# Kernel optimization log

Measured on AMD Instinct MI355X. Metric: run time of the kernel, lower is better.

Reference implementation:

```python
import jax, jax.numpy as jnp
import numpy as np

B, S, H, NH = 2, 2048, 1024, 16
HD = H // NH  # 64


def setup_inputs() -> dict:
    key = jax.random.key(0)
    ks = jax.random.split(key, 9)
    w = lambda k: jax.random.normal(k, (H, H), dtype=jnp.float32) * 0.02  # torch Linear weight [out,in]
    b = lambda k: jax.random.normal(k, (H,), dtype=jnp.float32) * 0.02
    return {
        "hidden_states": jax.random.normal(ks[0], (B, S, H), dtype=jnp.float32),
        "Wq": w(ks[1]), "bq": b(ks[2]),
        "Wk": w(ks[3]), "bk": b(ks[4]),
        "Wv": w(ks[5]), "bv": b(ks[6]),
        "Wo": w(ks[7]), "bo": b(ks[8]),
    }


def reference(hidden_states, Wq, bq, Wk, bk, Wv, bv, Wo, bo):
    b, s, h = hidden_states.shape
    nh, hd = NH, h // NH

    def proj(W, bias):
        y = hidden_states @ W.T + bias  # torch Linear: x W^T + b
        return y.reshape(b, s, nh, hd).transpose(0, 2, 1, 3)  # [b, h, s, d]

    q = proj(Wq, bq)
    k = proj(Wk, bk)
    v = proj(Wv, bv)

    scale = jnp.sqrt(jnp.asarray(hd, dtype=q.dtype))
    scores = jnp.einsum("bhqd,bhkd->bhqk", q, k) / scale  # [b, h, s, s]
    pos = jnp.arange(s)
    causal = pos[:, None] < pos[None, :]  # True where masked (key after query)
    scores = jnp.where(causal[None, None], -jnp.inf, scores)
    attn = jax.nn.softmax(scores, axis=-1)
    out = jnp.einsum("bhqk,bhkd->bhqd", attn, v)
    out = out.transpose(0, 2, 1, 3).reshape(b, s, h)
    return out @ Wo.T + bo
```

## Files before the change

kernel.cpp:

```cpp
#include <hip/hip_runtime.h>
#include <stdint.h>

typedef __bf16 bf16;
typedef __attribute__((ext_vector_type(2))) __bf16 bf16x2;
typedef __attribute__((ext_vector_type(4))) __bf16 bf16x4;
typedef __attribute__((ext_vector_type(8))) __bf16 bf16x8;
typedef __attribute__((ext_vector_type(4))) float f32x4;
typedef __attribute__((ext_vector_type(4))) short s16x4;

#define B_  2
#define S_  2048
#define H_  1024
#define NH_ 16
#define HD_ 64

__device__ __forceinline__ void glds16(const bf16* g, bf16* l) {
  __builtin_amdgcn_global_load_lds(
      (const __attribute__((address_space(1))) uint32_t*)g,
      (__attribute__((address_space(3))) uint32_t*)l, 16, 0, 0);
}

__device__ __forceinline__ f32x4 pv_mfma(bf16x4 a, bf16x4 b, f32x4 c) {
#if __has_builtin(__builtin_amdgcn_mfma_f32_16x16x16bf16_1k)
  union U { bf16x4 h; s16x4 s; };
  U ua; ua.h = a;
  U ub; ub.h = b;
  return __builtin_amdgcn_mfma_f32_16x16x16bf16_1k(ua.s, ub.s, c, 0, 0, 0);
#else
  f32x4 d;
  asm volatile("v_mfma_f32_16x16x16_bf16 %0, %1, %2, %3\n\ts_nop 7\n\ts_nop 7"
               : "=v"(d) : "v"(a), "v"(b), "v"(c));
  return d;
#endif
}

__global__ __launch_bounds__(256) void cvt_f32_bf16(
    const float* __restrict__ s0, bf16* __restrict__ d0, int n0,
    const float* __restrict__ s1, bf16* __restrict__ d1,
    const float* __restrict__ s2, bf16* __restrict__ d2,
    const float* __restrict__ s3, bf16* __restrict__ d3,
    const float* __restrict__ s4, bf16* __restrict__ d4, int nw)
{
  const float* s; bf16* d; int n;
  switch (blockIdx.y) {
    case 0:  s = s0; d = d0; n = n0; break;
    case 1:  s = s1; d = d1; n = nw; break;
    case 2:  s = s2; d = d2; n = nw; break;
    case 3:  s = s3; d = d3; n = nw; break;
    default: s = s4; d = d4; n = nw; break;
  }
  const int i = (blockIdx.x * 256 + threadIdx.x) * 8;
  if (i >= n) return;
  float4 v0 = *(const float4*)(s + i);
  float4 v1 = *(const float4*)(s + i + 4);
  bf16x8 o;
  o[0] = (bf16)v0.x; o[1] = (bf16)v0.y; o[2] = (bf16)v0.z; o[3] = (bf16)v0.w;
  o[4] = (bf16)v1.x; o[5] = (bf16)v1.y; o[6] = (bf16)v1.z; o[7] = (bf16)v1.w;
  *(bf16x8*)(d + i) = o;
}

__global__ __launch_bounds__(256) void gemm_qkv(
    const bf16* __restrict__ X,
    const bf16* __restrict__ W0, const bf16* __restrict__ W1, const bf16* __restrict__ W2,
    const float* __restrict__ b0, const float* __restrict__ b1, const float* __restrict__ b2,
    bf16* __restrict__ Y0, bf16* __restrict__ Y1, bf16* __restrict__ Y2,
    float ys0, int M, int N, int K)
{
  const bf16* W; const float* bias; bf16* Y; float ysc;
  if (blockIdx.z == 0)      { W = W0; bias = b0; Y = Y0; ysc = ys0; }
  else if (blockIdx.z == 1) { W = W1; bias = b1; Y = Y1; ysc = 1.0f; }
  else                      { W = W2; bias = b2; Y = Y2; ysc = 1.0f; }

  __shared__ __align__(16) bf16 As[2][128 * 32];
  __shared__ __align__(16) bf16 Bs[2][128 * 32];

  const int tid  = threadIdx.x;
  const int lane = tid & 63;
  const int wave = tid >> 6;
  const int m0 = blockIdx.y * 128;
  const int n0 = blockIdx.x * 128;
  const int wm = (wave >> 1) * 64;
  const int wn = (wave & 1) * 64;

  const int r0 = tid >> 2,            c0 = (tid & 3) * 8;
  const int r1 = (256 + tid) >> 2,    c1 = ((256 + tid) & 3) * 8;
  const int cb0 = (wave * 64) * 8;
  const int cb1 = (256 + wave * 64) * 8;

  f32x4 acc[4][4] = {};

  glds16(X + (size_t)(m0 + r0) * K + c0, &As[0][cb0]);
  glds16(W + (size_t)(n0 + r0) * K + c0, &Bs[0][cb0]);
  glds16(X + (size_t)(m0 + r1) * K + c1, &As[0][cb1]);
  glds16(W + (size_t)(n0 + r1) * K + c1, &Bs[0][cb1]);

  int pb = 0;
  for (int k0 = 0; k0 < K; k0 += 32, pb ^= 1) {
    __syncthreads();

    if (k0 + 32 < K) {
      const int kn = k0 + 32;
      glds16(X + (size_t)(m0 + r0) * K + kn + c0, &As[pb ^ 1][cb0]);
      glds16(W + (size_t)(n0 + r0) * K + kn + c0, &Bs[pb ^ 1][cb0]);
      glds16(X + (size_t)(m0 + r1) * K + kn + c1, &As[pb ^ 1][cb1]);
      glds16(W + (size_t)(n0 + r1) * K + kn + c1, &Bs[pb ^ 1][cb1]);
    }

    bf16x8 a[4], b[4];
#pragma unroll
    for (int i = 0; i < 4; ++i)
      a[i] = *(const bf16x8*)&As[pb][(wm + i * 16 + (lane & 15)) * 32 + (lane >> 4) * 8];
#pragma unroll
    for (int i = 0; i < 4; ++i)
      b[i] = *(const bf16x8*)&Bs[pb][(wn + i * 16 + (lane & 15)) * 32 + (lane >> 4) * 8];
#pragma unroll
    for (int mi = 0; mi < 4; ++mi)
#pragma unroll
      for (int ni = 0; ni < 4; ++ni)
        acc[mi][ni] = __builtin_amdgcn_mfma_f32_16x16x32_bf16(a[mi], b[ni], acc[mi][ni], 0, 0, 0);
  }

#pragma unroll
  for (int mi = 0; mi < 4; ++mi) {
    const int row = m0 + wm + mi * 16 + (lane >> 4) * 4;
#pragma unroll
    for (int ni = 0; ni < 4; ++ni) {
      const int col = n0 + wn + ni * 16 + (lane & 15);
      const float bv = bias[col];
#pragma unroll
      for (int r = 0; r < 4; ++r)
        Y[(size_t)(row + r) * N + col] = (bf16)((acc[mi][ni][r] + bv) * ysc);
    }
  }
}

__global__ __launch_bounds__(256) void gemm_o_64(
    const bf16* __restrict__ X, const bf16* __restrict__ W,
    const float* __restrict__ bias, float* __restrict__ Y)
{
  constexpr int K = 1024, N = 1024;
  __shared__ __align__(16) bf16 As[2][64 * 32];
  __shared__ __align__(16) bf16 Bs[2][128 * 32];

  const int tid  = threadIdx.x;
  const int lane = tid & 63;
  const int wave = tid >> 6;
  const int m0 = blockIdx.y * 64;
  const int n0 = blockIdx.x * 128;
  const int wm = (wave >> 1) * 32;
  const int wn = (wave & 1) * 64;

  const int ar = tid >> 2,  ac = (tid & 3) * 8;
  const int br0 = tid >> 2,          bc0 = (tid & 3) * 8;
  const int br1 = (256 + tid) >> 2,  bc1 = ((256 + tid) & 3) * 8;
  const int acb  = (wave * 64) * 8;
  const int bcb0 = (wave * 64) * 8;
  const int bcb1 = (256 + wave * 64) * 8;

  f32x4 acc[2][4] = {};

  glds16(X + (size_t)(m0 + ar) * K + ac,   &As[0][acb]);
  glds16(W + (size_t)(n0 + br0) * K + bc0, &Bs[0][bcb0]);
  glds16(W + (size_t)(n0 + br1) * K + bc1, &Bs[0][bcb1]);

  int pb = 0;
  for (int k0 = 0; k0 < K; k0 += 32, pb ^= 1) {
    __syncthreads();

    if (k0 + 32 < K) {
      const int kn = k0 + 32;
      glds16(X + (size_t)(m0 + ar) * K + kn + ac,   &As[pb ^ 1][acb]);
      glds16(W + (size_t)(n0 + br0) * K + kn + bc0, &Bs[pb ^ 1][bcb0]);
      glds16(W + (size_t)(n0 + br1) * K + kn + bc1, &Bs[pb ^ 1][bcb1]);
    }

    bf16x8 a[2], b[4];
#pragma unroll
    for (int i = 0; i < 2; ++i)
      a[i] = *(const bf16x8*)&As[pb][(wm + i * 16 + (lane & 15)) * 32 + (lane >> 4) * 8];
#pragma unroll
    for (int i = 0; i < 4; ++i)
      b[i] = *(const bf16x8*)&Bs[pb][(wn + i * 16 + (lane & 15)) * 32 + (lane >> 4) * 8];
#pragma unroll
    for (int mi = 0; mi < 2; ++mi)
#pragma unroll
      for (int ni = 0; ni < 4; ++ni)
        acc[mi][ni] = __builtin_amdgcn_mfma_f32_16x16x32_bf16(a[mi], b[ni], acc[mi][ni], 0, 0, 0);
  }

#pragma unroll
  for (int mi = 0; mi < 2; ++mi) {
    const int row = m0 + wm + mi * 16 + (lane >> 4) * 4;
#pragma unroll
    for (int ni = 0; ni < 4; ++ni) {
      const int col = n0 + wn + ni * 16 + (lane & 15);
      const float bv = bias[col];
#pragma unroll
      for (int r = 0; r < 4; ++r)
        Y[(size_t)(row + r) * N + col] = acc[mi][ni][r] + bv;
    }
  }
}

__device__ __forceinline__ void attn_tile_step(
    const bf16* Ksb, const bf16* Vtb, const bf16x8 bq[2], int qrow, int k0,
    bool maskit, float& mr, float& lr, f32x4 oacc[4], int l15, int quad)
{
  f32x4 sacc[8] = {};
  __builtin_amdgcn_s_setprio(1);
#pragma unroll
  for (int ks = 0; ks < 2; ++ks) {
#pragma unroll
    for (int mb = 0; mb < 8; ++mb) {
      const int row = mb * 16 + l15;
      const int ch  = (ks * 4 + quad) ^ (l15 & 7);
      bf16x8 ak = *(const bf16x8*)&Ksb[row * 64 + ch * 8];
      sacc[mb] = __builtin_amdgcn_mfma_f32_16x16x32_bf16(ak, bq[ks], sacc[mb], 0, 0, 0);
    }
  }
  __builtin_amdgcn_s_setprio(0);

  if (maskit) {
#pragma unroll
    for (int mb = 0; mb < 8; ++mb) {
      const int kb = k0 + mb * 16 + quad * 4;
#pragma unroll
      for (int r = 0; r < 4; ++r)
        if (kb + r > qrow) sacc[mb][r] = -1e30f;
    }
  }

  float mx = -1e30f;
#pragma unroll
  for (int mb = 0; mb < 8; ++mb)
    mx = fmaxf(mx, fmaxf(fmaxf(sacc[mb][0], sacc[mb][1]),
                         fmaxf(sacc[mb][2], sacc[mb][3])));
  mx = fmaxf(mx, __shfl_xor(mx, 16, 64));
  mx = fmaxf(mx, __shfl_xor(mx, 32, 64));

  float sum = 0.0f;
  bf16x4 pwv[8];
#pragma unroll
  for (int mb = 0; mb < 8; ++mb) {
    bf16x4 pw;
#pragma unroll
    for (int r = 0; r < 4; ++r) {
      const float p = __builtin_amdgcn_exp2f(sacc[mb][r] - mr);
      sum += p;
      pw[r] = (bf16)p;
    }
    pwv[mb] = pw;
  }
  sum += __shfl_xor(sum, 16, 64);
  sum += __shfl_xor(sum, 32, 64);

  __builtin_amdgcn_s_setprio(1);
#pragma unroll
  for (int mb = 0; mb < 8; ++mb) {
#pragma unroll
    for (int db = 0; db < 4; ++db) {
      const int vch = ((mb * 4 + quad) ^ (l15 & 7)) * 4;
      bf16x4 av = *(const bf16x4*)&Vtb[(db * 16 + l15) * 128 + vch];
      oacc[db] = pv_mfma(av, pwv[mb], oacc[db]);
    }
  }
  __builtin_amdgcn_s_setprio(0);

  lr += sum;
  if (!__all(mx <= mr + 8.0f)) {
    const float mnew  = fmaxf(mr, mx);
    const float alpha = __builtin_amdgcn_exp2f(mr - mnew);
    lr *= alpha;
#pragma unroll
    for (int db = 0; db < 4; ++db)
#pragma unroll
      for (int r = 0; r < 4; ++r) oacc[db][r] *= alpha;
    mr = mnew;
  }
}

__global__ __launch_bounds__(256, 2) void attn_causal(
    const bf16* __restrict__ Q, const bf16* __restrict__ K,
    const bf16* __restrict__ V, bf16* __restrict__ O)
{
  const int lin  = blockIdx.x;
  const int slot = lin >> 3;
  const int bh   = (lin & 7) * 4 + (slot >> 4);
  const int pair = slot & 15;
  const int b    = bh >> 4;
  const int h    = bh & 15;

  const int tid  = threadIdx.x;
  const int lane = tid & 63;
  const int wave = tid >> 6;
  const int quad = lane >> 4;
  const int l15  = lane & 15;
  const size_t headoff = (size_t)b * S_ * H_ + (size_t)h * HD_;
  const bf16* Kp = K + headoff;
  const bf16* Vp = V + headoff;

  __shared__ __align__(16) bf16 Ks[2][128 * 64];
  __shared__ __align__(16) bf16 Vt[2][64 * 128];

  const int qlo = pair, qhi = 31 - pair;
  const int nl  = (qlo >> 1) + 1;
  const int nh  = (qhi >> 1) + 1;
  const int qrowL = qlo * 64 + wave * 16 + l15;
  const int qrowH = qhi * 64 + wave * 16 + l15;

  bf16x8 bqL[2], bqH[2];
  bqL[0] = *(const bf16x8*)(Q + headoff + (size_t)qrowL * H_ + quad * 8);
  bqL[1] = *(const bf16x8*)(Q + headoff + (size_t)qrowL * H_ + 32 + quad * 8);
  bqH[0] = *(const bf16x8*)(Q + headoff + (size_t)qrowH * H_ + quad * 8);
  bqH[1] = *(const bf16x8*)(Q + headoff + (size_t)qrowH * H_ + 32 + quad * 8);

  const int vr = lane * 2;
  const int vc = wave * 16;

#define STAGE_K(k0_, buf_)                                                  \
  {                                                                         \
    _Pragma("unroll")                                                       \
    for (int j = 0; j < 4; ++j) {                                           \
      const int n = j * 256 + tid;                                          \
      const int row = n >> 3;                                               \
      const int cg  = (n & 7) ^ (row & 7);                                  \
      glds16(Kp + (size_t)((k0_) + row) * H_ + cg * 8,                      \
             &Ks[buf_][(j * 256 + wave * 64) * 8]);                         \
    }                                                                       \
  }

#define LOAD_V(k0_)                                                         \
  {                                                                         \
    vreg[0] = *(const bf16x8*)(Vp + (size_t)((k0_) + vr) * H_ + vc);        \
    vreg[1] = *(const bf16x8*)(Vp + (size_t)((k0_) + vr) * H_ + vc + 8);    \
    vreg[2] = *(const bf16x8*)(Vp + (size_t)((k0_) + vr + 1) * H_ + vc);    \
    vreg[3] = *(const bf16x8*)(Vp + (size_t)((k0_) + vr + 1) * H_ + vc + 8);\
  }

#define WRITE_V(buf_)                                                       \
  {                                                                         \
    _Pragma("unroll")                                                       \
    for (int e = 0; e < 8; ++e) {                                           \
      const int sw = (((vr >> 2) ^ e) * 4) + (vr & 3);                      \
      bf16x2 p0; p0[0] = vreg[0][e]; p0[1] = vreg[2][e];                    \
      *(bf16x2*)&Vt[buf_][(vc + e) * 128 + sw] = p0;                        \
      bf16x2 p1; p1[0] = vreg[1][e]; p1[1] = vreg[3][e];                    \
      *(bf16x2*)&Vt[buf_][(vc + 8 + e) * 128 + sw] = p1;                    \
    }                                                                       \
  }

  bf16x8 vreg[4];

  STAGE_K(0, 0);
  LOAD_V(0);
  WRITE_V(0);
  __syncthreads();

  float mrL = 0.0f, lrL = 0.0f, mrH = 0.0f, lrH = 0.0f;
  f32x4 oL[4] = {}, oH[4] = {};

  for (int it = 0; it < nh; ++it) {
    const int c = it & 1;
    const bool pre = (it + 1 < nh);

    if (pre) {
      STAGE_K((it + 1) * 128, c ^ 1);
      LOAD_V((it + 1) * 128);
    }

    attn_tile_step(Ks[c], Vt[c], bqH, qrowH, it * 128, it == nh - 1,
                   mrH, lrH, oH, l15, quad);
    if (it < nl)
      attn_tile_step(Ks[c], Vt[c], bqL, qrowL, it * 128, it == nl - 1,
                     mrL, lrL, oL, l15, quad);

    if (pre) {
      WRITE_V(c ^ 1);
      __syncthreads();
    }
  }

  const float invL = 1.0f / lrL;
#pragma unroll
  for (int db = 0; db < 4; ++db) {
    bf16x4 o;
#pragma unroll
    for (int r = 0; r < 4; ++r) o[r] = (bf16)(oL[db][r] * invL);
    *(bf16x4*)(O + headoff + (size_t)qrowL * H_ + db * 16 + quad * 4) = o;
  }
  const float invH = 1.0f / lrH;
#pragma unroll
  for (int db = 0; db < 4; ++db) {
    bf16x4 o;
#pragma unroll
    for (int r = 0; r < 4; ++r) o[r] = (bf16)(oH[db][r] * invH);
    *(bf16x4*)(O + headoff + (size_t)qrowH * H_ + db * 16 + quad * 4) = o;
  }
#undef STAGE_K
#undef LOAD_V
#undef WRITE_V
}

extern "C" void kernel_launch(void* const* d_in, const int* in_sizes, int n_in,
                              void* d_out, int out_size, void* d_ws, size_t ws_size,
                              hipStream_t stream) {
  const float* hs = (const float*)d_in[0];
  const float* Wq = (const float*)d_in[1]; const float* bq = (const float*)d_in[2];
  const float* Wk = (const float*)d_in[3]; const float* bk = (const float*)d_in[4];
  const float* Wv = (const float*)d_in[5]; const float* bv = (const float*)d_in[6];
  const float* Wo = (const float*)d_in[7]; const float* bo = (const float*)d_in[8];
  float* out = (float*)d_out;

  const size_t elems = (size_t)B_ * S_ * H_;
  const size_t wel   = (size_t)H_ * H_;
  bf16* hsb = (bf16*)d_ws;
  bf16* AO  = hsb;
  bf16* Wqb = hsb + elems;
  bf16* Wkb = Wqb + wel;
  bf16* Wvb = Wkb + wel;
  bf16* Wob = Wvb + wel;
  bf16* Qw  = Wob + wel;
  bf16* Kw  = Qw + elems;
  bf16* Vw  = Kw + elems;

  cvt_f32_bf16<<<dim3(2048, 5), dim3(256), 0, stream>>>(
      hs, hsb, (int)elems, Wq, Wqb, Wk, Wkb, Wv, Wvb, Wo, Wob, (int)wel);

  const int M = B_ * S_;
  const float QSCL = 0.125f * 1.44269504f;

  gemm_qkv<<<dim3(H_ / 128, M / 128, 3), dim3(256), 0, stream>>>(
      hsb, Wqb, Wkb, Wvb, bq, bk, bv, Qw, Kw, Vw, QSCL, M, H_, H_);

  attn_causal<<<dim3(512), dim3(256), 0, stream>>>(Qw, Kw, Vw, AO);

  gemm_o_64<<<dim3(8, 64), dim3(256), 0, stream>>>(AO, Wob, bo, out);
}
```

Measured before the change: 199.0 us.

## Fuse all four stages into one cooperative persistent kernel with grid syncs

Merges the conversion, QKV projection, causal attention and output projection into a single cooperatively launched kernel of 512 blocks, separated by grid-wide barriers. This removes three kernel launch boundaries and their tail gaps. The cost is that every phase must use one block count, one 64 KB shared-memory allocation and one register budget, and the QKV GEMM runs unevenly at 768 tiles over 512 blocks. If the cooperative launch fails, it falls back to four separate kernels.

```diff
diff --git a/kernel.cpp b/kernel.cpp
--- a/kernel.cpp
+++ b/kernel.cpp
@@ -1,5 +1,8 @@
 #include <hip/hip_runtime.h>
+#include <hip/hip_cooperative_groups.h>
 #include <stdint.h>
+
+namespace cg = cooperative_groups;
 
 typedef __bf16 bf16;
 typedef __attribute__((ext_vector_type(2))) __bf16 bf16x2;
@@ -13,6 +16,7 @@
 #define H_  1024
 #define NH_ 16
 #define HD_ 64
+#define QSCL_ (0.125f * 1.44269504f)
 
 __device__ __forceinline__ void glds16(const bf16* g, bf16* l) {
   __builtin_amdgcn_global_load_lds(
@@ -34,85 +38,92 @@
 #endif
 }
 
-__global__ __launch_bounds__(256) void cvt_f32_bf16(
-    const float* __restrict__ s0, bf16* __restrict__ d0, int n0,
-    const float* __restrict__ s1, bf16* __restrict__ d1,
-    const float* __restrict__ s2, bf16* __restrict__ d2,
-    const float* __restrict__ s3, bf16* __restrict__ d3,
-    const float* __restrict__ s4, bf16* __restrict__ d4, int nw)
-{
-  const float* s; bf16* d; int n;
-  switch (blockIdx.y) {
-    case 0:  s = s0; d = d0; n = n0; break;
-    case 1:  s = s1; d = d1; n = nw; break;
-    case 2:  s = s2; d = d2; n = nw; break;
-    case 3:  s = s3; d = d3; n = nw; break;
-    default: s = s4; d = d4; n = nw; break;
-  }
-  const int i = (blockIdx.x * 256 + threadIdx.x) * 8;
-  if (i >= n) return;
-  float4 v0 = *(const float4*)(s + i);
-  float4 v1 = *(const float4*)(s + i + 4);
+__device__ __forceinline__ bf16x8 cvt8(const float4 a, const float4 b) {
   bf16x8 o;
-  o[0] = (bf16)v0.x; o[1] = (bf16)v0.y; o[2] = (bf16)v0.z; o[3] = (bf16)v0.w;
-  o[4] = (bf16)v1.x; o[5] = (bf16)v1.y; o[6] = (bf16)v1.z; o[7] = (bf16)v1.w;
-  *(bf16x8*)(d + i) = o;
-}
-
-__global__ __launch_bounds__(256) void gemm_qkv(
+  o[0] = (bf16)a.x; o[1] = (bf16)a.y; o[2] = (bf16)a.z; o[3] = (bf16)a.w;
+  o[4] = (bf16)b.x; o[5] = (bf16)b.y; o[6] = (bf16)b.z; o[7] = (bf16)b.w;
+  return o;
+}
+
+
+__device__ __forceinline__ void cvt_phase(
+    int blk, int tid,
+    const float* __restrict__ hs, const float* __restrict__ Wq,
+    const float* __restrict__ Wk, const float* __restrict__ Wv,
+    const float* __restrict__ Wo,
+    bf16* __restrict__ hsb, bf16* __restrict__ Wqb, bf16* __restrict__ Wkb,
+    bf16* __restrict__ Wvb, bf16* __restrict__ Wob)
+{
+  const int g = blk * 256 + tid;
+#pragma unroll
+  for (int j = 0; j < 4; ++j) {
+    const size_t i = ((size_t)g + (size_t)j * 131072) * 8;
+    float4 a = *(const float4*)(hs + i), b = *(const float4*)(hs + i + 4);
+    *(bf16x8*)(hsb + i) = cvt8(a, b);
+  }
+  const size_t i = (size_t)g * 8;
+  { float4 a = *(const float4*)(Wq + i), b = *(const float4*)(Wq + i + 4);
+    *(bf16x8*)(Wqb + i) = cvt8(a, b); }
+  { float4 a = *(const float4*)(Wk + i), b = *(const float4*)(Wk + i + 4);
+    *(bf16x8*)(Wkb + i) = cvt8(a, b); }
+  { float4 a = *(const float4*)(Wv + i), b = *(const float4*)(Wv + i + 4);
+    *(bf16x8*)(Wvb + i) = cvt8(a, b); }
+  { float4 a = *(const float4*)(Wo + i), b = *(const float4*)(Wo + i + 4);
+    *(bf16x8*)(Wob + i) = cvt8(a, b); }
+}
+
+__device__ __forceinline__ void qkv_tile(
+    int z, int by, int bx, int tid, bf16* __restrict__ SM,
     const bf16* __restrict__ X,
     const bf16* __restrict__ W0, const bf16* __restrict__ W1, const bf16* __restrict__ W2,
     const float* __restrict__ b0, const float* __restrict__ b1, const float* __restrict__ b2,
-    bf16* __restrict__ Y0, bf16* __restrict__ Y1, bf16* __restrict__ Y2,
-    float ys0, int M, int N, int K)
-{
+    bf16* __restrict__ Y0, bf16* __restrict__ Y1, bf16* __restrict__ Y2)
+{
+  constexpr int K = 1024, N = 1024;
   const bf16* W; const float* bias; bf16* Y; float ysc;
-  if (blockIdx.z == 0)      { W = W0; bias = b0; Y = Y0; ysc = ys0; }
-  else if (blockIdx.z == 1) { W = W1; bias = b1; Y = Y1; ysc = 1.0f; }
-  else                      { W = W2; bias = b2; Y = Y2; ysc = 1.0f; }
-
-  __shared__ __align__(16) bf16 As[2][128 * 32];
-  __shared__ __align__(16) bf16 Bs[2][128 * 32];
-
-  const int tid  = threadIdx.x;
-  const int lane = tid & 63;
-  const int wave = tid >> 6;
-  const int m0 = blockIdx.y * 128;
-  const int n0 = blockIdx.x * 128;
-  const int wm = (wave >> 1) * 64;
-  const int wn = (wave & 1) * 64;
-
-  const int r0 = tid >> 2,            c0 = (tid & 3) * 8;
-  const int r1 = (256 + tid) >> 2,    c1 = ((256 + tid) & 3) * 8;
-  const int cb0 = (wave * 64) * 8;
-  const int cb1 = (256 + wave * 64) * 8;
+  if (z == 0)      { W = W0; bias = b0; Y = Y0; ysc = QSCL_; }
+  else if (z == 1) { W = W1; bias = b1; Y = Y1; ysc = 1.0f; }
+  else             { W = W2; bias = b2; Y = Y2; ysc = 1.0f; }
+
+  const int lane = tid & 63, wave = tid >> 6;
+  const int m0 = by * 128, n0 = bx * 128;
+  const int wm = (wave >> 1) * 64, wn = (wave & 1) * 64;
+  const int r0 = tid >> 2,         c0 = (tid & 3) * 8;
+  const int r1 = (256 + tid) >> 2, c1 = ((256 + tid) & 3) * 8;
+  const int cb0 = (wave * 64) * 8, cb1 = (256 + wave * 64) * 8;
+
+  bf16* As = SM;
+  bf16* Bs = SM + 8192;
 
   f32x4 acc[4][4] = {};
 
-  glds16(X + (size_t)(m0 + r0) * K + c0, &As[0][cb0]);
-  glds16(W + (size_t)(n0 + r0) * K + c0, &Bs[0][cb0]);
-  glds16(X + (size_t)(m0 + r1) * K + c1, &As[0][cb1]);
-  glds16(W + (size_t)(n0 + r1) * K + c1, &Bs[0][cb1]);
+  __syncthreads();
+  glds16(X + (size_t)(m0 + r0) * K + c0, As + cb0);
+  glds16(W + (size_t)(n0 + r0) * K + c0, Bs + cb0);
+  glds16(X + (size_t)(m0 + r1) * K + c1, As + cb1);
+  glds16(W + (size_t)(n0 + r1) * K + c1, Bs + cb1);
 
   int pb = 0;
   for (int k0 = 0; k0 < K; k0 += 32, pb ^= 1) {
     __syncthreads();
-
     if (k0 + 32 < K) {
       const int kn = k0 + 32;
-      glds16(X + (size_t)(m0 + r0) * K + kn + c0, &As[pb ^ 1][cb0]);
-      glds16(W + (size_t)(n0 + r0) * K + kn + c0, &Bs[pb ^ 1][cb0]);
-      glds16(X + (size_t)(m0 + r1) * K + kn + c1, &As[pb ^ 1][cb1]);
-      glds16(W + (size_t)(n0 + r1) * K + kn + c1, &Bs[pb ^ 1][cb1]);
-    }
-
+      bf16* An = As + (pb ^ 1) * 4096;
+      bf16* Bn = Bs + (pb ^ 1) * 4096;
+      glds16(X + (size_t)(m0 + r0) * K + kn + c0, An + cb0);
+      glds16(W + (size_t)(n0 + r0) * K + kn + c0, Bn + cb0);
+      glds16(X + (size_t)(m0 + r1) * K + kn + c1, An + cb1);
+      glds16(W + (size_t)(n0 + r1) * K + kn + c1, Bn + cb1);
+    }
+    const bf16* Ac = As + pb * 4096;
+    const bf16* Bc = Bs + pb * 4096;
     bf16x8 a[4], b[4];
 #pragma unroll
-    for (int i = 0; i < 4; ++i)
-      a[i] = *(const bf16x8*)&As[pb][(wm + i * 16 + (lane & 15)) * 32 + (lane >> 4) * 8];
-#pragma unroll
-    for (int i = 0; i < 4; ++i)
-      b[i] = *(const bf16x8*)&Bs[pb][(wn + i * 16 + (lane & 15)) * 32 + (lane >> 4) * 8];
+    for (int j = 0; j < 4; ++j)
+      a[j] = *(const bf16x8*)&Ac[(wm + j * 16 + (lane & 15)) * 32 + (lane >> 4) * 8];
+#pragma unroll
+    for (int j = 0; j < 4; ++j)
+      b[j] = *(const bf16x8*)&Bc[(wn + j * 16 + (lane & 15)) * 32 + (lane >> 4) * 8];
 #pragma unroll
     for (int mi = 0; mi < 4; ++mi)
 #pragma unroll
@@ -134,22 +145,16 @@
   }
 }
 
-__global__ __launch_bounds__(256) void gemm_o_64(
+__device__ __forceinline__ void o_tile(
+    int t, int tid, bf16* __restrict__ SM,
     const bf16* __restrict__ X, const bf16* __restrict__ W,
     const float* __restrict__ bias, float* __restrict__ Y)
 {
   constexpr int K = 1024, N = 1024;
-  __shared__ __align__(16) bf16 As[2][64 * 32];
-  __shared__ __align__(16) bf16 Bs[2][128 * 32];
-
-  const int tid  = threadIdx.x;
-  const int lane = tid & 63;
-  const int wave = tid >> 6;
-  const int m0 = blockIdx.y * 64;
-  const int n0 = blockIdx.x * 128;
-  const int wm = (wave >> 1) * 32;
-  const int wn = (wave & 1) * 64;
-
+  const int lane = tid & 63, wave = tid >> 6;
+  const int m0 = (t >> 3) * 64;
+  const int n0 = (t & 7) * 128;
+  const int wm = (wave >> 1) * 32, wn = (wave & 1) * 64;
   const int ar = tid >> 2,  ac = (tid & 3) * 8;
   const int br0 = tid >> 2,          bc0 = (tid & 3) * 8;
   const int br1 = (256 + tid) >> 2,  bc1 = ((256 + tid) & 3) * 8;
@@ -157,30 +162,36 @@
   const int bcb0 = (wave * 64) * 8;
   const int bcb1 = (256 + wave * 64) * 8;
 
+  bf16* As = SM;
+  bf16* Bs = SM + 4096;
+
   f32x4 acc[2][4] = {};
 
-  glds16(X + (size_t)(m0 + ar) * K + ac,   &As[0][acb]);
-  glds16(W + (size_t)(n0 + br0) * K + bc0, &Bs[0][bcb0]);
-  glds16(W + (size_t)(n0 + br1) * K + bc1, &Bs[0][bcb1]);
+  __syncthreads();
+  glds16(X + (size_t)(m0 + ar) * K + ac,   As + acb);
+  glds16(W + (size_t)(n0 + br0) * K + bc0, Bs + bcb0);
+  glds16(W + (size_t)(n0 + br1) * K + bc1, Bs + bcb1);
 
   int pb = 0;
   for (int k0 = 0; k0 < K; k0 += 32, pb ^= 1) {
     __syncthreads();
-
     if (k0 + 32 < K) {
       const int kn = k0 + 32;
-      glds16(X + (size_t)(m0 + ar) * K + kn + ac,   &As[pb ^ 1][acb]);
-      glds16(W + (size_t)(n0 + br0) * K + kn + bc0, &Bs[pb ^ 1][bcb0]);
-      glds16(W + (size_t)(n0 + br1) * K + kn + bc1, &Bs[pb ^ 1][bcb1]);
-    }
-
+      bf16* An = As + (pb ^ 1) * 2048;
+      bf16* Bn = Bs + (pb ^ 1) * 4096;
+      glds16(X + (size_t)(m0 + ar) * K + kn + ac,   An + acb);
+      glds16(W + (size_t)(n0 + br0) * K + kn + bc0, Bn + bcb0);
+      glds16(W + (size_t)(n0 + br1) * K + kn + bc1, Bn + bcb1);
+    }
+    const bf16* Ac = As + pb * 2048;
+    const bf16* Bc = Bs + pb * 4096;
     bf16x8 a[2], b[4];
 #pragma unroll
-    for (int i = 0; i < 2; ++i)
-      a[i] = *(const bf16x8*)&As[pb][(wm + i * 16 + (lane & 15)) * 32 + (lane >> 4) * 8];
-#pragma unroll
-    for (int i = 0; i < 4; ++i)
-      b[i] = *(const bf16x8*)&Bs[pb][(wn + i * 16 + (lane & 15)) * 32 + (lane >> 4) * 8];
+    for (int j = 0; j < 2; ++j)
+      a[j] = *(const bf16x8*)&Ac[(wm + j * 16 + (lane & 15)) * 32 + (lane >> 4) * 8];
+#pragma unroll
+    for (int j = 0; j < 4; ++j)
+      b[j] = *(const bf16x8*)&Bc[(wn + j * 16 + (lane & 15)) * 32 + (lane >> 4) * 8];
 #pragma unroll
     for (int mi = 0; mi < 2; ++mi)
 #pragma unroll
@@ -279,28 +290,24 @@
   }
 }
 
-__global__ __launch_bounds__(256, 2) void attn_causal(
+__device__ __forceinline__ void attn_block(
+    int lin, int tid, bf16* __restrict__ SM,
     const bf16* __restrict__ Q, const bf16* __restrict__ K,
     const bf16* __restrict__ V, bf16* __restrict__ O)
 {
-  const int lin  = blockIdx.x;
   const int slot = lin >> 3;
   const int bh   = (lin & 7) * 4 + (slot >> 4);
   const int pair = slot & 15;
   const int b    = bh >> 4;
   const int h    = bh & 15;
 
-  const int tid  = threadIdx.x;
-  const int lane = tid & 63;
-  const int wave = tid >> 6;
-  const int quad = lane >> 4;
-  const int l15  = lane & 15;
+  const int lane = tid & 63, wave = tid >> 6, quad = lane >> 4, l15 = lane & 15;
   const size_t headoff = (size_t)b * S_ * H_ + (size_t)h * HD_;
   const bf16* Kp = K + headoff;
   const bf16* Vp = V + headoff;
 
-  __shared__ __align__(16) bf16 Ks[2][128 * 64];
-  __shared__ __align__(16) bf16 Vt[2][64 * 128];
+  bf16* Ks = SM;
+  bf16* Vt = SM + 16384;
 
   const int qlo = pair, qhi = 31 - pair;
   const int nl  = (qlo >> 1) + 1;
@@ -325,7 +332,7 @@
       const int row = n >> 3;                                               \
       const int cg  = (n & 7) ^ (row & 7);                                  \
       glds16(Kp + (size_t)((k0_) + row) * H_ + cg * 8,                      \
-             &Ks[buf_][(j * 256 + wave * 64) * 8]);                         \
+             Ks + (buf_) * 8192 + (j * 256 + wave * 64) * 8);               \
     }                                                                       \
   }
 
@@ -343,9 +350,9 @@
     for (int e = 0; e < 8; ++e) {                                           \
       const int sw = (((vr >> 2) ^ e) * 4) + (vr & 3);                      \
       bf16x2 p0; p0[0] = vreg[0][e]; p0[1] = vreg[2][e];                    \
-      *(bf16x2*)&Vt[buf_][(vc + e) * 128 + sw] = p0;                        \
+      *(bf16x2*)&Vt[(buf_) * 8192 + (vc + e) * 128 + sw] = p0;              \
       bf16x2 p1; p1[0] = vreg[1][e]; p1[1] = vreg[3][e];                    \
-      *(bf16x2*)&Vt[buf_][(vc + 8 + e) * 128 + sw] = p1;                    \
+      *(bf16x2*)&Vt[(buf_) * 8192 + (vc + 8 + e) * 128 + sw] = p1;          \
     }                                                                       \
   }
 
@@ -368,11 +375,11 @@
       LOAD_V((it + 1) * 128);
     }
 
-    attn_tile_step(Ks[c], Vt[c], bqH, qrowH, it * 128, it == nh - 1,
-                   mrH, lrH, oH, l15, quad);
+    attn_tile_step(Ks + c * 8192, Vt + c * 8192, bqH, qrowH, it * 128,
+                   it == nh - 1, mrH, lrH, oH, l15, quad);
     if (it < nl)
-      attn_tile_step(Ks[c], Vt[c], bqL, qrowL, it * 128, it == nl - 1,
-                     mrL, lrL, oL, l15, quad);
+      attn_tile_step(Ks + c * 8192, Vt + c * 8192, bqL, qrowL, it * 128,
+                     it == nl - 1, mrL, lrL, oL, l15, quad);
 
     if (pre) {
       WRITE_V(c ^ 1);
@@ -399,6 +406,91 @@
 #undef STAGE_K
 #undef LOAD_V
 #undef WRITE_V
+}
+
+__global__ __launch_bounds__(256, 2) void mega(
+    const float* __restrict__ hs,
+    const float* __restrict__ Wq, const float* __restrict__ Wk,
+    const float* __restrict__ Wv, const float* __restrict__ Wo,
+    const float* __restrict__ bq, const float* __restrict__ bk,
+    const float* __restrict__ bv, const float* __restrict__ bo,
+    float* __restrict__ out, bf16* __restrict__ ws)
+{
+  __shared__ __align__(16) bf16 SM[32768];
+  cg::grid_group grid = cg::this_grid();
+
+  const size_t elems = (size_t)B_ * S_ * H_;
+  const size_t wel   = (size_t)H_ * H_;
+  bf16* hsb = ws;
+  bf16* AO  = ws;
+  bf16* Wqb = ws + elems;
+  bf16* Wkb = Wqb + wel;
+  bf16* Wvb = Wkb + wel;
+  bf16* Wob = Wvb + wel;
+  bf16* Qw  = Wob + wel;
+  bf16* Kw  = Qw + elems;
+  bf16* Vw  = Kw + elems;
+
+  const int tid = threadIdx.x;
+  const int blk = blockIdx.x;
+
+  cvt_phase(blk, tid, hs, Wq, Wk, Wv, Wo, hsb, Wqb, Wkb, Wvb, Wob);
+  grid.sync();
+
+  for (int t = blk; t < 768; t += 512) {
+    const int z = t >> 8, r = t & 255;
+    qkv_tile(z, r >> 3, r & 7, tid, SM, hsb, Wqb, Wkb, Wvb,
+             bq, bk, bv, Qw, Kw, Vw);
+  }
+  grid.sync();
+
+  attn_block(blk, tid, SM, Qw, Kw, Vw, AO);
+  grid.sync();
+
+  o_tile(blk, tid, SM, AO, Wob, bo, out);
+}
+
+__global__ __launch_bounds__(256) void k_cvt(
+    const float* __restrict__ hs, const float* __restrict__ Wq,
+    const float* __restrict__ Wk, const float* __restrict__ Wv,
+    const float* __restrict__ Wo, bf16* __restrict__ ws)
+{
+  const size_t elems = (size_t)B_ * S_ * H_;
+  const size_t wel   = (size_t)H_ * H_;
+  bf16* hsb = ws;
+  bf16* Wqb = ws + elems;
+  bf16* Wkb = Wqb + wel;
+  bf16* Wvb = Wkb + wel;
+  bf16* Wob = Wvb + wel;
+  cvt_phase(blockIdx.x, threadIdx.x, hs, Wq, Wk, Wv, Wo, hsb, Wqb, Wkb, Wvb, Wob);
+}
+
+__global__ __launch_bounds__(256) void k_qkv(
+    const bf16* __restrict__ X,
+    const bf16* __restrict__ W0, const bf16* __restrict__ W1, const bf16* __restrict__ W2,
+    const float* __restrict__ b0, const float* __restrict__ b1, const float* __restrict__ b2,
+    bf16* __restrict__ Y0, bf16* __restrict__ Y1, bf16* __restrict__ Y2)
+{
+  __shared__ __align__(16) bf16 SM[16384];
+  const int t = blockIdx.x;
+  qkv_tile(t >> 8, (t & 255) >> 3, t & 7, threadIdx.x, SM,
+           X, W0, W1, W2, b0, b1, b2, Y0, Y1, Y2);
+}
+
+__global__ __launch_bounds__(256, 2) void k_attn(
+    const bf16* __restrict__ Q, const bf16* __restrict__ K,
+    const bf16* __restrict__ V, bf16* __restrict__ O)
+{
+  __shared__ __align__(16) bf16 SM[32768];
+  attn_block(blockIdx.x, threadIdx.x, SM, Q, K, V, O);
+}
+
+__global__ __launch_bounds__(256) void k_o(
+    const bf16* __restrict__ X, const bf16* __restrict__ W,
+    const float* __restrict__ bias, float* __restrict__ Y)
+{
+  __shared__ __align__(16) bf16 SM[12288];
+  o_tile(blockIdx.x, threadIdx.x, SM, X, W, bias, Y);
 }
 
 extern "C" void kernel_launch(void* const* d_in, const int* in_sizes, int n_in,
@@ -410,29 +502,29 @@
   const float* Wv = (const float*)d_in[5]; const float* bv = (const float*)d_in[6];
   const float* Wo = (const float*)d_in[7]; const float* bo = (const float*)d_in[8];
   float* out = (float*)d_out;
-
-  const size_t elems = (size_t)B_ * S_ * H_;
-  const size_t wel   = (size_t)H_ * H_;
-  bf16* hsb = (bf16*)d_ws;
-  bf16* AO  = hsb;
-  bf16* Wqb = hsb + elems;
-  bf16* Wkb = Wqb + wel;
-  bf16* Wvb = Wkb + wel;
-  bf16* Wob = Wvb + wel;
-  bf16* Qw  = Wob + wel;
-  bf16* Kw  = Qw + elems;
-  bf16* Vw  = Kw + elems;
-
-  cvt_f32_bf16<<<dim3(2048, 5), dim3(256), 0, stream>>>(
-      hs, hsb, (int)elems, Wq, Wqb, Wk, Wkb, Wv, Wvb, Wo, Wob, (int)wel);
-
-  const int M = B_ * S_;
-  const float QSCL = 0.125f * 1.44269504f;
-
-  gemm_qkv<<<dim3(H_ / 128, M / 128, 3), dim3(256), 0, stream>>>(
-      hsb, Wqb, Wkb, Wvb, bq, bk, bv, Qw, Kw, Vw, QSCL, M, H_, H_);
-
-  attn_causal<<<dim3(512), dim3(256), 0, stream>>>(Qw, Kw, Vw, AO);
-
-  gemm_o_64<<<dim3(8, 64), dim3(256), 0, stream>>>(AO, Wob, bo, out);
-}
+  bf16* ws = (bf16*)d_ws;
+
+  void* args[] = {(void*)&hs, (void*)&Wq, (void*)&Wk, (void*)&Wv, (void*)&Wo,
+                  (void*)&bq, (void*)&bk, (void*)&bv, (void*)&bo,
+                  (void*)&out, (void*)&ws};
+
+  if (hipLaunchCooperativeKernel((const void*)mega, dim3(512), dim3(256),
+                                 args, 0, stream) != hipSuccess) {
+    const size_t elems = (size_t)B_ * S_ * H_;
+    const size_t wel   = (size_t)H_ * H_;
+    bf16* hsb = ws; bf16* AO = ws;
+    bf16* Wqb = ws + elems;
+    bf16* Wkb = Wqb + wel;
+    bf16* Wvb = Wkb + wel;
+    bf16* Wob = Wvb + wel;
+    bf16* Qw  = Wob + wel;
+    bf16* Kw  = Qw + elems;
+    bf16* Vw  = Kw + elems;
+
+    k_cvt<<<dim3(512), dim3(256), 0, stream>>>(hs, Wq, Wk, Wv, Wo, ws);
+    k_qkv<<<dim3(768), dim3(256), 0, stream>>>(hsb, Wqb, Wkb, Wvb,
+                                               bq, bk, bv, Qw, Kw, Vw);
+    k_attn<<<dim3(512), dim3(256), 0, stream>>>(Qw, Kw, Vw, AO);
+    k_o<<<dim3(512), dim3(256), 0, stream>>>(AO, Wob, bo, out);
+  }
+}
```

Result: slower. 398.6 us (+100.3%).
